# Kernel tuning notes

Measured on AMD Instinct MI355X. Metric: run time of the kernel, lower is better.

Reference implementation:

```python
import math
import jax, jax.numpy as jnp
import numpy as np

D_MODEL = 256
N_HEADS = 4
HEAD_DIM = D_MODEL // N_HEADS
MAX_REL = 30


def _rel_pos_encodings(t, d_model):
    # sinusoidal table over clipped relative distances -> [t, t, d_model]
    n = 2 * MAX_REL + 1
    positions = jnp.arange(n, dtype=jnp.float32)[:, None]
    div_term = jnp.exp(jnp.arange(0, d_model, 2, dtype=jnp.float32) * (-math.log(10000.0) / d_model))
    ang = positions * div_term                      # [n, d/2]
    enc = jnp.stack([jnp.sin(ang), jnp.cos(ang)], axis=-1).reshape(n, d_model)
    rng = jnp.arange(t)
    final_mat = jnp.clip(rng[None, :] - rng[:, None], -MAX_REL, MAX_REL) + MAX_REL  # [t, t]
    return enc[final_mat]                           # [t, t, d_model]


def setup_inputs() -> dict:
    key = jax.random.key(0)
    ks = jax.random.split(key, 12)
    d = D_MODEL
    s = 1.0 / math.sqrt(d)
    inp = {
        "inputs": jax.random.normal(ks[0], (16, 512, d), dtype=jnp.float32),
        "ln_gamma": jnp.ones((d,), jnp.float32),
        "ln_beta": jnp.zeros((d,), jnp.float32),
        "Wq": jax.random.normal(ks[1], (d, d), jnp.float32) * s,
        "bq": jnp.zeros((d,), jnp.float32),
        "Wk": jax.random.normal(ks[2], (d, d), jnp.float32) * s,
        "bk": jnp.zeros((d,), jnp.float32),
        "Wv": jax.random.normal(ks[3], (d, d), jnp.float32) * s,
        "bv": jnp.zeros((d,), jnp.float32),
        "Wpos": jax.random.normal(ks[4], (d, d), jnp.float32) * s,
        "bpos": jnp.zeros((d,), jnp.float32),
        "Wo": jax.random.normal(ks[5], (d, d), jnp.float32) * s,
        "bo": jnp.zeros((d,), jnp.float32),
        "u_bias": jax.random.normal(ks[6], (1, N_HEADS, 1, HEAD_DIM), jnp.float32) * 0.02,
        "v_bias": jax.random.normal(ks[7], (1, N_HEADS, 1, HEAD_DIM), jnp.float32) * 0.02,
    }
    return inp


def reference(inputs, ln_gamma, ln_beta, Wq, bq, Wk, bk, Wv, bv, Wpos, bpos, Wo, bo, u_bias, v_bias):
    b, t, d = inputs.shape
    h, hd = N_HEADS, HEAD_DIM
    # LayerNorm (eps=1e-5, torch default)
    mu = jnp.mean(inputs, axis=-1, keepdims=True)
    var = jnp.mean(jnp.square(inputs - mu), axis=-1, keepdims=True)
    x = (inputs - mu) * jax.lax.rsqrt(var + 1e-5) * ln_gamma + ln_beta

    def split_heads(y):
        return y.reshape(b, t, h, hd).transpose(0, 2, 1, 3)  # b h t d

    q = split_heads(x @ Wq.T + bq)
    k = split_heads(x @ Wk.T + bk)
    v = split_heads(x @ Wv.T + bv)

    rel = jax.lax.stop_gradient(_rel_pos_encodings(t, d))    # [t, t, d]
    pos = (rel @ Wpos.T + bpos).reshape(t, t, h, hd)         # [t1, t2, h, hd]

    qk_score = jnp.einsum('bhtd,bhsd->bhts', q + u_bias, k)
    pos_score = jnp.einsum('bhtd,tshd->bhts', q + v_bias, pos)
    scores = (qk_score + pos_score) / math.sqrt(hd)
    attn = jax.nn.softmax(scores, axis=-1)
    ctx = jnp.einsum('bhts,bhsd->bhtd', attn, v)
    ctx = ctx.transpose(0, 2, 1, 3).reshape(b, t, d)
    return ctx @ Wo.T + bo
```

## Files before the change

### kernel.cpp

```cpp
#include <hip/hip_runtime.h>
#include <hip/hip_bf16.h>
#include <math.h>

#define B 16
#define T 512
#define D 256
#define H 4
#define HD 64
#define MAXREL 30
#define NREL 61
#define M_ROWS (B*T)
#define QBLK 128

typedef __attribute__((ext_vector_type(8))) short bf16x8;
typedef __attribute__((ext_vector_type(4))) float f32x4;
typedef unsigned short ush;

__device__ inline ush f2b(float f) {
    __hip_bfloat16 h = __float2bfloat16(f);
    union { __hip_bfloat16 h; ush u; } c; c.h = h; return c.u;
}
__device__ inline float b2f(ush u) {
    union { ush u; __hip_bfloat16 h; } c; c.u = u; return __bfloat162float(c.h);
}
__device__ inline unsigned int pk2(float a, float b) {
    __hip_bfloat162 h = __float22bfloat162_rn(make_float2(a, b));
    union { __hip_bfloat162 h; unsigned int u; } c; c.h = h; return c.u;
}
__device__ inline int swz(int row, int byteoff) {
    return row * 128 + (byteoff ^ ((row & 7) << 4));
}
__device__ inline int swz256(int row, int byteoff) {
    return row * 256 + (byteoff ^ ((row & 7) << 4));
}
__device__ inline int swz512(int row, int byteoff) {
    return row * 512 + (byteoff ^ ((row & 7) << 4));
}

#define SCL 0.1803368801111204f

__global__ __launch_bounds__(256) void prep_kernel(const float* __restrict__ x,
                                                   const float* __restrict__ gamma,
                                                   const float* __restrict__ beta,
                                                   ush* __restrict__ xb,
                                                   const float* __restrict__ Wq, const float* __restrict__ Wk,
                                                   const float* __restrict__ Wv, const float* __restrict__ Wo,
                                                   ush* __restrict__ wb,
                                                   const float* __restrict__ Wpos,
                                                   const float* __restrict__ bpos,
                                                   ush* __restrict__ pospb) {
    __shared__ __attribute__((aligned(16))) ush wpS[64 * 256];
    int bid = blockIdx.x;
    int tid = threadIdx.x;
    if (bid < 512) {
        int lane = tid & 63;
        float4 g = *(const float4*)(gamma + lane * 4);
        float4 bb = *(const float4*)(beta + lane * 4);
        #pragma unroll
        for (int it = 0; it < 4; ++it) {
            int row = bid * 16 + it * 4 + (tid >> 6);
            const float* xr = x + (size_t)row * D;
            float4 v = *(const float4*)(xr + lane * 4);
            float s = v.x + v.y + v.z + v.w;
            #pragma unroll
            for (int off = 32; off; off >>= 1) s += __shfl_xor(s, off);
            float mu = s * (1.f / 256.f);
            float dx = v.x - mu, dy = v.y - mu, dz = v.z - mu, dw = v.w - mu;
            float vs = dx*dx + dy*dy + dz*dz + dw*dw;
            #pragma unroll
            for (int off = 32; off; off >>= 1) vs += __shfl_xor(vs, off);
            float rstd = rsqrtf(vs * (1.f / 256.f) + 1e-5f);
            ushort4 o;
            o.x = f2b(dx * rstd * g.x + bb.x);
            o.y = f2b(dy * rstd * g.y + bb.y);
            o.z = f2b(dz * rstd * g.z + bb.z);
            o.w = f2b(dw * rstd * g.w + bb.w);
            *(ushort4*)(xb + (size_t)row * D + lane * 4) = o;
        }
    } else if (bid < 512 + 256) {
        int b2 = bid - 512;
        int z = b2 >> 6, xblk = b2 & 63;
        const float* src = z == 0 ? Wq : z == 1 ? Wk : z == 2 ? Wv : Wo;
        int idx = (xblk * 256 + tid) * 4;
        float4 v = *(const float4*)(src + idx);
        ushort4 o;
        o.x = f2b(v.x); o.y = f2b(v.y); o.z = f2b(v.z); o.w = f2b(v.w);
        *(ushort4*)(wb + (size_t)z * 65536 + idx) = o;
    } else {
        int h = bid - 768;
        int w = tid >> 6, l = tid & 63, lg = l >> 4, ln = l & 15;
        const float* wsrc = Wpos + (size_t)(h * 64) * D;
        #pragma unroll
        for (int c = 0; c < 16; ++c) {
            int idx = c * 256 + tid;
            int row = idx >> 6, col = (idx & 63) * 4;
            float4 v = *(const float4*)(wsrc + (size_t)row * D + col);
            ushort4 o; o.x = f2b(v.x); o.y = f2b(v.y); o.z = f2b(v.z); o.w = f2b(v.w);
            *(ushort4*)((char*)wpS + swz512(row, col * 2)) = o;
        }
        int p = w * 16 + ln;
        bf16x8 af[8];
        #pragma unroll
        for (int ks = 0; ks < 8; ++ks) {
            #pragma unroll
            for (int j = 0; j < 8; ++j) {
                int k = ks * 32 + lg * 8 + j;
                int i = k >> 1;
                float dt = __expf(-(2.f * i) * (9.210340371976184f / 256.f));
                float ang = (float)p * dt;
                float v = (k & 1) ? __cosf(ang) : __sinf(ang);
                af[ks][j] = (short)f2b(v);
            }
        }
        __syncthreads();
        f32x4 acc[4] = {};
        #pragma unroll
        for (int ks = 0; ks < 8; ++ks) {
            int kbyte = (ks * 32 + lg * 8) * 2;
            #pragma unroll
            for (int ct = 0; ct < 4; ++ct) {
                bf16x8 bf = *(const bf16x8*)((const char*)wpS + swz512(ct * 16 + ln, kbyte));
                acc[ct] = __builtin_amdgcn_mfma_f32_16x16x32_bf16(af[ks], bf, acc[ct], 0, 0, 0);
            }
        }
        #pragma unroll
        for (int ct = 0; ct < 4; ++ct) {
            int dcol = ct * 16 + ln;
            float bb = bpos[h * 64 + dcol];
            #pragma unroll
            for (int r = 0; r < 4; ++r) {
                int pr = w * 16 + lg * 4 + r;
                pospb[(size_t)h * 4096 + pr * 64 + dcol] = f2b(acc[ct][r] + bb);
            }
        }
    }
}

__global__ __launch_bounds__(256, 3) void qkv_mfma(const ush* __restrict__ A,
                                                   const ush* __restrict__ wball,
                                                   const float* __restrict__ bq,
                                                   const float* __restrict__ bk,
                                                   const float* __restrict__ bv,
                                                   ush* __restrict__ qb,
                                                   ush* __restrict__ kbuf,
                                                   ush* __restrict__ vtb) {
    __shared__ __attribute__((aligned(16))) ush A_s[128 * 128];
    __shared__ __attribute__((aligned(16))) ush B_s[64 * 128];
    int tid = threadIdx.x;
    int w = tid >> 6, l = tid & 63;
    int lg = l >> 4, ln = l & 15;
    int wr = w >> 1, wc = w & 1;
    int i0 = blockIdx.x * 128;
    int j0 = blockIdx.y * 64;
    int z = blockIdx.z;
    const ush* Wp = wball + (size_t)z * 65536 + (size_t)j0 * D;
    const ush* Ap = A + (size_t)i0 * D;
    const float* bias = z == 0 ? bq : (z == 1 ? bk : bv);
    f32x4 acc[2][4] = {};

    #pragma unroll 1
    for (int kb2 = 0; kb2 < 2; ++kb2) {
        int k0 = kb2 * 128;
        if (kb2) __syncthreads();
        #pragma unroll
        for (int c = 0; c < 8; ++c) {
            int u = c * 256 + tid;
            int row = u >> 4, sub = u & 15;
            *(bf16x8*)((char*)A_s + swz256(row, sub * 16)) = *(const bf16x8*)(Ap + (size_t)row * D + k0 + sub * 8);
        }
        #pragma unroll
        for (int c = 0; c < 4; ++c) {
            int u = c * 256 + tid;
            int row = u >> 4, sub = u & 15;
            *(bf16x8*)((char*)B_s + swz256(row, sub * 16)) = *(const bf16x8*)(Wp + (size_t)row * D + k0 + sub * 8);
        }
        __syncthreads();
        __builtin_amdgcn_s_setprio(1);
        #pragma unroll
        for (int ksub = 0; ksub < 4; ++ksub) {
            int kbyte = ksub * 64 + lg * 16;
            bf16x8 af[2], bfr[4];
            #pragma unroll
            for (int mi = 0; mi < 2; ++mi)
                af[mi] = *(const bf16x8*)((const char*)B_s + swz256(wr * 32 + mi * 16 + ln, kbyte));
            #pragma unroll
            for (int ni = 0; ni < 4; ++ni)
                bfr[ni] = *(const bf16x8*)((const char*)A_s + swz256(wc * 64 + ni * 16 + ln, kbyte));
            #pragma unroll
            for (int mi = 0; mi < 2; ++mi)
                #pragma unroll
                for (int ni = 0; ni < 4; ++ni)
                    acc[mi][ni] = __builtin_amdgcn_mfma_f32_16x16x32_bf16(af[mi], bfr[ni], acc[mi][ni], 0, 0, 0);
        }
        __builtin_amdgcn_s_setprio(0);
    }

    if (z == 2) {
        #pragma unroll
        for (int mi = 0; mi < 2; ++mi) {
            int jb = j0 + wr * 32 + mi * 16 + lg * 4;
            float4 bv4 = *(const float4*)(bias + jb);
            float bvv[4] = {bv4.x, bv4.y, bv4.z, bv4.w};
            #pragma unroll
            for (int ni = 0; ni < 4; ++ni) {
                int t = i0 + wc * 64 + ni * 16 + ln;
                #pragma unroll
                for (int r = 0; r < 4; ++r)
                    vtb[(size_t)(jb + r) * M_ROWS + t] = f2b(acc[mi][ni][r] + bvv[r]);
            }
        }
    } else {
        ush* ob = (z == 0) ? qb : kbuf;
        #pragma unroll
        for (int mi = 0; mi < 2; ++mi) {
            int jb = j0 + wr * 32 + mi * 16 + lg * 4;
            float4 bv4 = *(const float4*)(bias + jb);
            #pragma unroll
            for (int ni = 0; ni < 4; ++ni) {
                int t = i0 + wc * 64 + ni * 16 + ln;
                ushort4 o;
                o.x = f2b(acc[mi][ni][0] + bv4.x); o.y = f2b(acc[mi][ni][1] + bv4.y);
                o.z = f2b(acc[mi][ni][2] + bv4.z); o.w = f2b(acc[mi][ni][3] + bv4.w);
                *(ushort4*)(ob + (size_t)t * D + jb) = o;
            }
        }
    }
}

__global__ __launch_bounds__(256, 2) void outproj_mfma(const ush* __restrict__ A,
                                                       const ush* __restrict__ W,
                                                       const float* __restrict__ bias,
                                                       float* __restrict__ of) {
    __shared__ __attribute__((aligned(16))) ush A_s[64 * 128];
    __shared__ __attribute__((aligned(16))) ush B_s[64 * 128];
    int tid = threadIdx.x;
    int w = tid >> 6, l = tid & 63;
    int lg = l >> 4, ln = l & 15;
    int wr = w >> 1, wc = w & 1;
    int i0 = blockIdx.x * 64;
    int j0 = blockIdx.y * 64;
    const ush* Ap = A + (size_t)i0 * D;
    const ush* Wp = W + (size_t)j0 * D;
    f32x4 acc[2][2] = {};

    #pragma unroll 1
    for (int kb2 = 0; kb2 < 2; ++kb2) {
        int k0 = kb2 * 128;
        if (kb2) __syncthreads();
        #pragma unroll
        for (int c = 0; c < 4; ++c) {
            int u = c * 256 + tid;
            int row = u >> 4, sub = u & 15;
            *(bf16x8*)((char*)A_s + swz256(row, sub * 16)) = *(const bf16x8*)(Ap + (size_t)row * D + k0 + sub * 8);
            *(bf16x8*)((char*)B_s + swz256(row, sub * 16)) = *(const bf16x8*)(Wp + (size_t)row * D + k0 + sub * 8);
        }
        __syncthreads();
        __builtin_amdgcn_s_setprio(1);
        #pragma unroll
        for (int ksub = 0; ksub < 4; ++ksub) {
            int kbyte = ksub * 64 + lg * 16;
            bf16x8 af[2], bfr[2];
            #pragma unroll
            for (int mi = 0; mi < 2; ++mi)
                af[mi] = *(const bf16x8*)((const char*)B_s + swz256(wr * 32 + mi * 16 + ln, kbyte));
            #pragma unroll
            for (int ni = 0; ni < 2; ++ni)
                bfr[ni] = *(const bf16x8*)((const char*)A_s + swz256(wc * 32 + ni * 16 + ln, kbyte));
            #pragma unroll
            for (int mi = 0; mi < 2; ++mi)
                #pragma unroll
                for (int ni = 0; ni < 2; ++ni)
                    acc[mi][ni] = __builtin_amdgcn_mfma_f32_16x16x32_bf16(af[mi], bfr[ni], acc[mi][ni], 0, 0, 0);
        }
        __builtin_amdgcn_s_setprio(0);
    }

    #pragma unroll
    for (int mi = 0; mi < 2; ++mi) {
        int jb = j0 + wr * 32 + mi * 16 + lg * 4;
        float4 bv4 = *(const float4*)(bias + jb);
        #pragma unroll
        for (int ni = 0; ni < 2; ++ni) {
            int t = i0 + wc * 32 + ni * 16 + ln;
            float4 o;
            o.x = acc[mi][ni][0] + bv4.x; o.y = acc[mi][ni][1] + bv4.y;
            o.z = acc[mi][ni][2] + bv4.z; o.w = acc[mi][ni][3] + bv4.w;
            *(float4*)(of + (size_t)t * D + jb) = o;
        }
    }
}

__global__ __launch_bounds__(512, 2) void attn_mfma(const ush* __restrict__ qb,
                                                    const ush* __restrict__ kb,
                                                    const ush* __restrict__ vtb,
                                                    const ush* __restrict__ pospb,
                                                    const float* __restrict__ u_bias,
                                                    const float* __restrict__ v_bias,
                                                    ush* __restrict__ ctxb) {
    __shared__ __attribute__((aligned(16))) ush Kd[4][64 * 64];
    __shared__ __attribute__((aligned(16))) ush Vd[4][64 * 64];
    __shared__ __attribute__((aligned(16))) ush pdS[8][16 * 66];
    __shared__ __attribute__((aligned(16))) ush PlS[8][16 * 64];

    int tid = threadIdx.x;
    int w = tid >> 6;
    int l = tid & 63;
    int lg = l >> 4, ln = l & 15;
    int bh = blockIdx.x;
    int b = bh >> 2, h = bh & 3;
    int t0 = blockIdx.y * QBLK;
    const size_t baseBH = ((size_t)b * T) * D + h * HD;

    bf16x8 qu[2], qv[2];
    {
        const ush* qrow = qb + baseBH + (size_t)(t0 + w * 16 + ln) * D;
        int c0 = lg * 8;
        #pragma unroll
        for (int ks = 0; ks < 2; ++ks) {
            bf16x8 ld = *(const bf16x8*)(qrow + ks * 32 + c0);
            float4 ub0 = *(const float4*)(u_bias + h * HD + ks * 32 + c0);
            float4 ub1 = *(const float4*)(u_bias + h * HD + ks * 32 + c0 + 4);
            float4 vb0 = *(const float4*)(v_bias + h * HD + ks * 32 + c0);
            float4 vb1 = *(const float4*)(v_bias + h * HD + ks * 32 + c0 + 4);
            float ubv[8] = {ub0.x,ub0.y,ub0.z,ub0.w,ub1.x,ub1.y,ub1.z,ub1.w};
            float vbv[8] = {vb0.x,vb0.y,vb0.z,vb0.w,vb1.x,vb1.y,vb1.z,vb1.w};
            #pragma unroll
            for (int j = 0; j < 8; ++j) {
                float f = b2f((ush)ld[j]);
                qu[ks][j] = (short)f2b((f + ubv[j]) * SCL);
                qv[ks][j] = (short)f2b((f + vbv[j]) * SCL);
            }
        }
    }

    int r0 = tid >> 3, c0 = tid & 7;
    const ush* kbase = kb + baseBH;
    const ush* vbase = vtb + (size_t)(h * HD) * M_ROWS + (size_t)b * T;
    const ush* pbase = pospb + (size_t)h * 4096;

    {
        bf16x8 pp0 = *(const bf16x8*)(pbase + r0 * 64 + c0 * 8);
        bf16x8 k0 = *(const bf16x8*)(kbase + (size_t)r0 * D + c0 * 8);
        bf16x8 k1 = *(const bf16x8*)(kbase + (size_t)(64 + r0) * D + c0 * 8);
        bf16x8 v0 = *(const bf16x8*)(vbase + (size_t)r0 * M_ROWS + c0 * 8);
        bf16x8 v1 = *(const bf16x8*)(vbase + (size_t)r0 * M_ROWS + 64 + c0 * 8);
        *(bf16x8*)((char*)Kd[2] + swz(r0, c0 * 16)) = pp0;
        *(bf16x8*)((char*)Kd[0] + swz(r0, c0 * 16)) = k0;
        *(bf16x8*)((char*)Kd[1] + swz(r0, c0 * 16)) = k1;
        *(bf16x8*)((char*)Vd[0] + swz(r0, c0 * 16)) = v0;
        *(bf16x8*)((char*)Vd[1] + swz(r0, c0 * 16)) = v1;
    }
    bf16x8 sk0 = *(const bf16x8*)(kbase + (size_t)(128 + r0) * D + c0 * 8);
    bf16x8 sk1 = *(const bf16x8*)(kbase + (size_t)(192 + r0) * D + c0 * 8);
    bf16x8 sv0 = *(const bf16x8*)(vbase + (size_t)r0 * M_ROWS + 128 + c0 * 8);
    bf16x8 sv1 = *(const bf16x8*)(vbase + (size_t)r0 * M_ROWS + 192 + c0 * 8);
    __syncthreads();

    ush* pdW = pdS[w];
    {
        f32x4 pacc[4] = {};
        #pragma unroll
        for (int ks = 0; ks < 2; ++ks)
            #pragma unroll
            for (int ct = 0; ct < 4; ++ct) {
                bf16x8 bf = *(const bf16x8*)((const char*)Kd[2] + swz(ct * 16 + ln, (ks * 32 + lg * 8) * 2));
                pacc[ct] = __builtin_amdgcn_mfma_f32_16x16x32_bf16(qv[ks], bf, pacc[ct], 0, 0, 0);
            }
        #pragma unroll
        for (int ct = 0; ct < 4; ++ct)
            #pragma unroll
            for (int r = 0; r < 4; ++r)
                pdW[(lg * 4 + r) * 66 + ct * 16 + ln] = f2b(pacc[ct][r]);
    }
    float pdlo = b2f(pdW[ln * 66 + 0]);
    float pdhi = b2f(pdW[ln * 66 + 60]);
    __syncthreads();

    f32x4 lacc = {};
    f32x4 o_acc[4] = {};
    ush* pw = PlS[w];
    bf16x8 ones;
    #pragma unroll
    for (int j = 0; j < 8; ++j) ones[j] = (short)0x3F80;

    #pragma unroll 1
    for (int it = 0; it < 4; ++it) {
        int cb = (it & 1) * 2;
        int ob = cb ^ 2;
        if (it < 3) {
            *(bf16x8*)((char*)Kd[ob] + swz(r0, c0 * 16)) = sk0;
            *(bf16x8*)((char*)Kd[ob + 1] + swz(r0, c0 * 16)) = sk1;
            *(bf16x8*)((char*)Vd[ob] + swz(r0, c0 * 16)) = sv0;
            *(bf16x8*)((char*)Vd[ob + 1] + swz(r0, c0 * 16)) = sv1;
        }
        if (it < 2) {
            int sn = it * 128 + 256;
            sk0 = *(const bf16x8*)(kbase + (size_t)(sn + r0) * D + c0 * 8);
            sk1 = *(const bf16x8*)(kbase + (size_t)(sn + 64 + r0) * D + c0 * 8);
            sv0 = *(const bf16x8*)(vbase + (size_t)r0 * M_ROWS + sn + c0 * 8);
            sv1 = *(const bf16x8*)(vbase + (size_t)r0 * M_ROWS + sn + 64 + c0 * 8);
        }

        #pragma unroll
        for (int tt = 0; tt < 2; ++tt) {
            int s0 = (2 * it + tt) * 64;
            const char* Kc = (const char*)Kd[cb + tt];
            const char* Vc = (const char*)Vd[cb + tt];

            int dlt = s0 - t0;
            float cinit;
            if (dlt >= 192) cinit = pdhi;
            else if (dlt <= -128) cinit = pdlo;
            else cinit = 0.f;
            f32x4 sacc[4];
            #pragma unroll
            for (int ct = 0; ct < 4; ++ct)
                #pragma unroll
                for (int r = 0; r < 4; ++r) sacc[ct][r] = cinit;

            __builtin_amdgcn_s_setprio(1);
            #pragma unroll
            for (int ks = 0; ks < 2; ++ks)
                #pragma unroll
                for (int ct = 0; ct < 4; ++ct) {
                    bf16x8 kf = *(const bf16x8*)(Kc + swz(ct * 16 + ln, (ks * 32 + lg * 8) * 2));
                    sacc[ct] = __builtin_amdgcn_mfma_f32_16x16x32_bf16(kf, qu[ks], sacc[ct], 0, 0, 0);
                }
            __builtin_amdgcn_s_setprio(0);

            if (dlt > -128 && dlt < 192) {
                int t_glob = t0 + w * 16 + ln;
                #pragma unroll
                for (int ct = 0; ct < 4; ++ct) {
                    #pragma unroll
                    for (int r = 0; r < 4; ++r) {
                        int s_g = s0 + ct * 16 + lg * 4 + r;
                        int rel = s_g - t_glob;
                        rel = rel < -MAXREL ? -MAXREL : (rel > MAXREL ? MAXREL : rel);
                        sacc[ct][r] += b2f(pdW[ln * 66 + rel + MAXREL]);
                    }
                }
            }

            #pragma unroll
            for (int ct = 0; ct < 4; ++ct)
                #pragma unroll
                for (int r = 0; r < 4; ++r)
                    sacc[ct][r] = exp2f(sacc[ct][r]);

            #pragma unroll
            for (int ct = 0; ct < 4; ++ct)
                #pragma unroll
                for (int rr = 0; rr < 2; ++rr)
                    *(unsigned int*)((char*)pw + swz(ln, (ct * 16 + lg * 4 + rr * 2) * 2)) =
                        pk2(sacc[ct][rr * 2], sacc[ct][rr * 2 + 1]);

            __builtin_amdgcn_s_setprio(1);
            #pragma unroll
            for (int ks = 0; ks < 2; ++ks) {
                bf16x8 pa = *(const bf16x8*)((const char*)pw + swz(ln, (ks * 32 + lg * 8) * 2));
                #pragma unroll
                for (int cd = 0; cd < 4; ++cd) {
                    bf16x8 bv8 = *(const bf16x8*)(Vc + swz(cd * 16 + ln, (ks * 32 + lg * 8) * 2));
                    o_acc[cd] = __builtin_amdgcn_mfma_f32_16x16x32_bf16(pa, bv8, o_acc[cd], 0, 0, 0);
                }
                lacc = __builtin_amdgcn_mfma_f32_16x16x32_bf16(pa, ones, lacc, 0, 0, 0);
            }
            __builtin_amdgcn_s_setprio(0);
        }

        __syncthreads();
    }

    float inv[4];
    #pragma unroll
    for (int r = 0; r < 4; ++r) inv[r] = 1.f / lacc[r];
    #pragma unroll
    for (int cd = 0; cd < 4; ++cd)
        #pragma unroll
        for (int r = 0; r < 4; ++r) {
            int t_loc = w * 16 + lg * 4 + r;
            ctxb[baseBH + (size_t)(t0 + t_loc) * D + cd * 16 + ln] = f2b(o_acc[cd][r] * inv[r]);
        }
}

extern "C" void kernel_launch(void* const* d_in, const int* in_sizes, int n_in,
                              void* d_out, int out_size, void* d_ws, size_t ws_size,
                              hipStream_t stream) {
    const float* inputs  = (const float*)d_in[0];
    const float* ln_g    = (const float*)d_in[1];
    const float* ln_b    = (const float*)d_in[2];
    const float* Wq      = (const float*)d_in[3];
    const float* bq      = (const float*)d_in[4];
    const float* Wk      = (const float*)d_in[5];
    const float* bk      = (const float*)d_in[6];
    const float* Wv      = (const float*)d_in[7];
    const float* bv      = (const float*)d_in[8];
    const float* Wpos    = (const float*)d_in[9];
    const float* bpos    = (const float*)d_in[10];
    const float* Wo      = (const float*)d_in[11];
    const float* bo      = (const float*)d_in[12];
    const float* u_bias  = (const float*)d_in[13];
    const float* v_bias  = (const float*)d_in[14];
    float* out = (float*)d_out;

    char* w = (char*)d_ws;
    ush* xb    = (ush*)w;  w += (size_t)M_ROWS * D * 2;
    ush* qb    = (ush*)w;  w += (size_t)M_ROWS * D * 2;
    ush* kbuf  = (ush*)w;  w += (size_t)M_ROWS * D * 2;
    ush* vtb   = (ush*)w;  w += (size_t)M_ROWS * D * 2;
    ush* ctxb  = (ush*)w;  w += (size_t)M_ROWS * D * 2;
    ush* wb    = (ush*)w;  w += (size_t)4 * 65536 * 2;
    ush* pospb = (ush*)w;  w += (size_t)4 * 64 * 64 * 2;

    prep_kernel<<<512 + 256 + 4, 256, 0, stream>>>(inputs, ln_g, ln_b, xb,
                                                   Wq, Wk, Wv, Wo, wb,
                                                   Wpos, bpos, pospb);

    qkv_mfma<<<dim3(M_ROWS / 128, 4, 3), 256, 0, stream>>>(xb, wb, bq, bk, bv, qb, kbuf, vtb);

    attn_mfma<<<dim3(B * H, T / QBLK), 512, 0, stream>>>(qb, kbuf, vtb, pospb, u_bias, v_bias, ctxb);

    outproj_mfma<<<dim3(M_ROWS / 64, 4), 256, 0, stream>>>(ctxb, wb + 3 * 65536, bo, out);
}
```

Before: 40.61 us.

## Convert weights to bf16 inside GEMM loads and move pos-proj into QKV launch

Drops the separate pass that converts weights to bf16. The QKV and output-projection GEMMs now read fp32 weights and convert them while staging into shared memory. The relative-position projection moves from the prep kernel into extra z=3 blocks of the QKV launch, so the prep kernel only does LayerNorm. This cuts a weight round-trip through global memory and makes the prep kernel lighter, but each GEMM block re-reads and re-converts fp32 weights (twice the bytes), and the z=3 slice launches many blocks that exit immediately.

```diff
diff --git a/kernel.cpp b/kernel.cpp
--- a/kernel.cpp
+++ b/kernel.cpp
@@ -36,111 +36,60 @@
 __device__ inline int swz512(int row, int byteoff) {
     return row * 512 + (byteoff ^ ((row & 7) << 4));
 }
+__device__ inline bf16x8 cvt8(const float* p) {
+    float4 a = *(const float4*)p, b = *(const float4*)(p + 4);
+    bf16x8 o;
+    o[0] = (short)f2b(a.x); o[1] = (short)f2b(a.y);
+    o[2] = (short)f2b(a.z); o[3] = (short)f2b(a.w);
+    o[4] = (short)f2b(b.x); o[5] = (short)f2b(b.y);
+    o[6] = (short)f2b(b.z); o[7] = (short)f2b(b.w);
+    return o;
+}
 
 #define SCL 0.1803368801111204f
 
-__global__ __launch_bounds__(256) void prep_kernel(const float* __restrict__ x,
-                                                   const float* __restrict__ gamma,
-                                                   const float* __restrict__ beta,
-                                                   ush* __restrict__ xb,
-                                                   const float* __restrict__ Wq, const float* __restrict__ Wk,
-                                                   const float* __restrict__ Wv, const float* __restrict__ Wo,
-                                                   ush* __restrict__ wb,
-                                                   const float* __restrict__ Wpos,
-                                                   const float* __restrict__ bpos,
-                                                   ush* __restrict__ pospb) {
-    __shared__ __attribute__((aligned(16))) ush wpS[64 * 256];
+__global__ __launch_bounds__(256) void ln_kernel(const float* __restrict__ x,
+                                                 const float* __restrict__ gamma,
+                                                 const float* __restrict__ beta,
+                                                 ush* __restrict__ xb) {
     int bid = blockIdx.x;
     int tid = threadIdx.x;
-    if (bid < 512) {
-        int lane = tid & 63;
-        float4 g = *(const float4*)(gamma + lane * 4);
-        float4 bb = *(const float4*)(beta + lane * 4);
-        #pragma unroll
-        for (int it = 0; it < 4; ++it) {
-            int row = bid * 16 + it * 4 + (tid >> 6);
-            const float* xr = x + (size_t)row * D;
-            float4 v = *(const float4*)(xr + lane * 4);
-            float s = v.x + v.y + v.z + v.w;
-            #pragma unroll
-            for (int off = 32; off; off >>= 1) s += __shfl_xor(s, off);
-            float mu = s * (1.f / 256.f);
-            float dx = v.x - mu, dy = v.y - mu, dz = v.z - mu, dw = v.w - mu;
-            float vs = dx*dx + dy*dy + dz*dz + dw*dw;
-            #pragma unroll
-            for (int off = 32; off; off >>= 1) vs += __shfl_xor(vs, off);
-            float rstd = rsqrtf(vs * (1.f / 256.f) + 1e-5f);
-            ushort4 o;
-            o.x = f2b(dx * rstd * g.x + bb.x);
-            o.y = f2b(dy * rstd * g.y + bb.y);
-            o.z = f2b(dz * rstd * g.z + bb.z);
-            o.w = f2b(dw * rstd * g.w + bb.w);
-            *(ushort4*)(xb + (size_t)row * D + lane * 4) = o;
-        }
-    } else if (bid < 512 + 256) {
-        int b2 = bid - 512;
-        int z = b2 >> 6, xblk = b2 & 63;
-        const float* src = z == 0 ? Wq : z == 1 ? Wk : z == 2 ? Wv : Wo;
-        int idx = (xblk * 256 + tid) * 4;
-        float4 v = *(const float4*)(src + idx);
+    int lane = tid & 63;
+    float4 g = *(const float4*)(gamma + lane * 4);
+    float4 bb = *(const float4*)(beta + lane * 4);
+    #pragma unroll
+    for (int it = 0; it < 4; ++it) {
+        int row = bid * 16 + it * 4 + (tid >> 6);
+        const float* xr = x + (size_t)row * D;
+        float4 v = *(const float4*)(xr + lane * 4);
+        float s = v.x + v.y + v.z + v.w;
+        #pragma unroll
+        for (int off = 32; off; off >>= 1) s += __shfl_xor(s, off);
+        float mu = s * (1.f / 256.f);
+        float dx = v.x - mu, dy = v.y - mu, dz = v.z - mu, dw = v.w - mu;
+        float vs = dx*dx + dy*dy + dz*dz + dw*dw;
+        #pragma unroll
+        for (int off = 32; off; off >>= 1) vs += __shfl_xor(vs, off);
+        float rstd = rsqrtf(vs * (1.f / 256.f) + 1e-5f);
         ushort4 o;
-        o.x = f2b(v.x); o.y = f2b(v.y); o.z = f2b(v.z); o.w = f2b(v.w);
-        *(ushort4*)(wb + (size_t)z * 65536 + idx) = o;
-    } else {
-        int h = bid - 768;
-        int w = tid >> 6, l = tid & 63, lg = l >> 4, ln = l & 15;
-        const float* wsrc = Wpos + (size_t)(h * 64) * D;
-        #pragma unroll
-        for (int c = 0; c < 16; ++c) {
-            int idx = c * 256 + tid;
-            int row = idx >> 6, col = (idx & 63) * 4;
-            float4 v = *(const float4*)(wsrc + (size_t)row * D + col);
-            ushort4 o; o.x = f2b(v.x); o.y = f2b(v.y); o.z = f2b(v.z); o.w = f2b(v.w);
-            *(ushort4*)((char*)wpS + swz512(row, col * 2)) = o;
-        }
-        int p = w * 16 + ln;
-        bf16x8 af[8];
-        #pragma unroll
-        for (int ks = 0; ks < 8; ++ks) {
-            #pragma unroll
-            for (int j = 0; j < 8; ++j) {
-                int k = ks * 32 + lg * 8 + j;
-                int i = k >> 1;
-                float dt = __expf(-(2.f * i) * (9.210340371976184f / 256.f));
-                float ang = (float)p * dt;
-                float v = (k & 1) ? __cosf(ang) : __sinf(ang);
-                af[ks][j] = (short)f2b(v);
-            }
-        }
-        __syncthreads();
-        f32x4 acc[4] = {};
-        #pragma unroll
-        for (int ks = 0; ks < 8; ++ks) {
-            int kbyte = (ks * 32 + lg * 8) * 2;
-            #pragma unroll
-            for (int ct = 0; ct < 4; ++ct) {
-                bf16x8 bf = *(const bf16x8*)((const char*)wpS + swz512(ct * 16 + ln, kbyte));
-                acc[ct] = __builtin_amdgcn_mfma_f32_16x16x32_bf16(af[ks], bf, acc[ct], 0, 0, 0);
-            }
-        }
-        #pragma unroll
-        for (int ct = 0; ct < 4; ++ct) {
-            int dcol = ct * 16 + ln;
-            float bb = bpos[h * 64 + dcol];
-            #pragma unroll
-            for (int r = 0; r < 4; ++r) {
-                int pr = w * 16 + lg * 4 + r;
-                pospb[(size_t)h * 4096 + pr * 64 + dcol] = f2b(acc[ct][r] + bb);
-            }
-        }
+        o.x = f2b(dx * rstd * g.x + bb.x);
+        o.y = f2b(dy * rstd * g.y + bb.y);
+        o.z = f2b(dz * rstd * g.z + bb.z);
+        o.w = f2b(dw * rstd * g.w + bb.w);
+        *(ushort4*)(xb + (size_t)row * D + lane * 4) = o;
     }
 }
 
 __global__ __launch_bounds__(256, 3) void qkv_mfma(const ush* __restrict__ A,
-                                                   const ush* __restrict__ wball,
+                                                   const float* __restrict__ Wq,
+                                                   const float* __restrict__ Wk,
+                                                   const float* __restrict__ Wv,
                                                    const float* __restrict__ bq,
                                                    const float* __restrict__ bk,
                                                    const float* __restrict__ bv,
+                                                   const float* __restrict__ Wpos,
+                                                   const float* __restrict__ bpos,
+                                                   ush* __restrict__ pospb,
                                                    ush* __restrict__ qb,
                                                    ush* __restrict__ kbuf,
                                                    ush* __restrict__ vtb) {
@@ -149,11 +98,64 @@
     int tid = threadIdx.x;
     int w = tid >> 6, l = tid & 63;
     int lg = l >> 4, ln = l & 15;
+
+    if (blockIdx.z == 3) {
+        if (blockIdx.x != 0) return;
+        ush* wpS = A_s;
+        int h = blockIdx.y;
+        const float* wsrc = Wpos + (size_t)(h * 64) * D;
+        #pragma unroll
+        for (int c = 0; c < 16; ++c) {
+            int idx = c * 256 + tid;
+            int row = idx >> 6, col = (idx & 63) * 4;
+            float4 v = *(const float4*)(wsrc + (size_t)row * D + col);
+            ushort4 o; o.x = f2b(v.x); o.y = f2b(v.y); o.z = f2b(v.z); o.w = f2b(v.w);
+            *(ushort4*)((char*)wpS + swz512(row, col * 2)) = o;
+        }
+        int p = w * 16 + ln;
+        bf16x8 af[8];
+        #pragma unroll
+        for (int ks = 0; ks < 8; ++ks) {
+            #pragma unroll
+            for (int j = 0; j < 8; ++j) {
+                int k = ks * 32 + lg * 8 + j;
+                int i = k >> 1;
+                float dt = __expf(-(2.f * i) * (9.210340371976184f / 256.f));
+                float ang = (float)p * dt;
+                float v = (k & 1) ? __cosf(ang) : __sinf(ang);
+                af[ks][j] = (short)f2b(v);
+            }
+        }
+        __syncthreads();
+        f32x4 acc[4] = {};
+        #pragma unroll
+        for (int ks = 0; ks < 8; ++ks) {
+            int kbyte = (ks * 32 + lg * 8) * 2;
+            #pragma unroll
+            for (int ct = 0; ct < 4; ++ct) {
+                bf16x8 bf = *(const bf16x8*)((const char*)wpS + swz512(ct * 16 + ln, kbyte));
+                acc[ct] = __builtin_amdgcn_mfma_f32_16x16x32_bf16(af[ks], bf, acc[ct], 0, 0, 0);
+            }
+        }
+        #pragma unroll
+        for (int ct = 0; ct < 4; ++ct) {
+            int dcol = ct * 16 + ln;
+            float bb = bpos[h * 64 + dcol];
+            #pragma unroll
+            for (int r = 0; r < 4; ++r) {
+                int pr = w * 16 + lg * 4 + r;
+                pospb[(size_t)h * 4096 + pr * 64 + dcol] = f2b(acc[ct][r] + bb);
+            }
+        }
+        return;
+    }
+
     int wr = w >> 1, wc = w & 1;
     int i0 = blockIdx.x * 128;
     int j0 = blockIdx.y * 64;
     int z = blockIdx.z;
-    const ush* Wp = wball + (size_t)z * 65536 + (size_t)j0 * D;
+    const float* Wsel = z == 0 ? Wq : (z == 1 ? Wk : Wv);
+    const float* Wp = Wsel + (size_t)j0 * D;
     const ush* Ap = A + (size_t)i0 * D;
     const float* bias = z == 0 ? bq : (z == 1 ? bk : bv);
     f32x4 acc[2][4] = {};
@@ -172,7 +174,7 @@
         for (int c = 0; c < 4; ++c) {
             int u = c * 256 + tid;
             int row = u >> 4, sub = u & 15;
-            *(bf16x8*)((char*)B_s + swz256(row, sub * 16)) = *(const bf16x8*)(Wp + (size_t)row * D + k0 + sub * 8);
+            *(bf16x8*)((char*)B_s + swz256(row, sub * 16)) = cvt8(Wp + (size_t)row * D + k0 + sub * 8);
         }
         __syncthreads();
         __builtin_amdgcn_s_setprio(1);
@@ -228,7 +230,7 @@
 }
 
 __global__ __launch_bounds__(256, 2) void outproj_mfma(const ush* __restrict__ A,
-                                                       const ush* __restrict__ W,
+                                                       const float* __restrict__ W,
                                                        const float* __restrict__ bias,
                                                        float* __restrict__ of) {
     __shared__ __attribute__((aligned(16))) ush A_s[64 * 128];
@@ -240,7 +242,7 @@
     int i0 = blockIdx.x * 64;
     int j0 = blockIdx.y * 64;
     const ush* Ap = A + (size_t)i0 * D;
-    const ush* Wp = W + (size_t)j0 * D;
+    const float* Wp = W + (size_t)j0 * D;
     f32x4 acc[2][2] = {};
 
     #pragma unroll 1
@@ -252,7 +254,7 @@
             int u = c * 256 + tid;
             int row = u >> 4, sub = u & 15;
             *(bf16x8*)((char*)A_s + swz256(row, sub * 16)) = *(const bf16x8*)(Ap + (size_t)row * D + k0 + sub * 8);
-            *(bf16x8*)((char*)B_s + swz256(row, sub * 16)) = *(const bf16x8*)(Wp + (size_t)row * D + k0 + sub * 8);
+            *(bf16x8*)((char*)B_s + swz256(row, sub * 16)) = cvt8(Wp + (size_t)row * D + k0 + sub * 8);
         }
         __syncthreads();
         __builtin_amdgcn_s_setprio(1);
@@ -510,16 +512,14 @@
     ush* kbuf  = (ush*)w;  w += (size_t)M_ROWS * D * 2;
     ush* vtb   = (ush*)w;  w += (size_t)M_ROWS * D * 2;
     ush* ctxb  = (ush*)w;  w += (size_t)M_ROWS * D * 2;
-    ush* wb    = (ush*)w;  w += (size_t)4 * 65536 * 2;
     ush* pospb = (ush*)w;  w += (size_t)4 * 64 * 64 * 2;
 
-    prep_kernel<<<512 + 256 + 4, 256, 0, stream>>>(inputs, ln_g, ln_b, xb,
-                                                   Wq, Wk, Wv, Wo, wb,
-                                                   Wpos, bpos, pospb);
-
-    qkv_mfma<<<dim3(M_ROWS / 128, 4, 3), 256, 0, stream>>>(xb, wb, bq, bk, bv, qb, kbuf, vtb);
+    ln_kernel<<<512, 256, 0, stream>>>(inputs, ln_g, ln_b, xb);
+
+    qkv_mfma<<<dim3(M_ROWS / 128, 4, 4), 256, 0, stream>>>(xb, Wq, Wk, Wv, bq, bk, bv,
+                                                           Wpos, bpos, pospb, qb, kbuf, vtb);
 
     attn_mfma<<<dim3(B * H, T / QBLK), 512, 0, stream>>>(qb, kbuf, vtb, pospb, u_bias, v_bias, ctxb);
 
-    outproj_mfma<<<dim3(M_ROWS / 64, 4), 256, 0, stream>>>(ctxb, wb + 3 * 65536, bo, out);
-}
+    outproj_mfma<<<dim3(M_ROWS / 64, 4), 256, 0, stream>>>(ctxb, Wo, bo, out);
+}
```

New measurement: 44.34 us. 1.09x slower.
